# Optimization experiments

Hardware: AMD Instinct MI355X
Metric: run time of the kernel (lower is better)

The kernel has to match this reference:

```python
import jax, jax.numpy as jnp
import numpy as np

N = 4096            # nodes
LMAX = 6
NUM_COEF = (LMAX + 1) ** 2   # 49 SH coefficients
RES = 18            # S2 grid resolution (lat = lon = 18)
C = 128             # num_channels


def setup_inputs() -> dict:
    key = jax.random.key(0)
    k1, k2, k3, k4 = jax.random.split(key, 4)
    return {
        "inputs": jax.random.normal(k1, (N, NUM_COEF, 2 * C), dtype=jnp.float32),
        "scalars": jax.random.normal(k2, (N, 3 * C), dtype=jnp.float32),
        # SO3Grid projection matrices (precomputed SH-basis grids in the real module)
        "to_grid_mat": jax.random.normal(k3, (RES, RES, NUM_COEF), dtype=jnp.float32) / np.sqrt(NUM_COEF).astype(np.float32),
        "from_grid_mat": jax.random.normal(k4, (RES, RES, NUM_COEF), dtype=jnp.float32) / np.float32(RES),
    }


def reference(inputs, scalars, to_grid_mat, from_grid_mat):
    # inputs:  [N, (lmax+1)^2, 2C]; scalars: [N, 3C]
    n, k, c2 = inputs.shape
    s = scalars[:, None, :]                       # [N, 1, 3C]
    # Type-0 path part 1: SwiGLU on first 2C scalars -> [N, 1, C]
    a, b = jnp.split(s[..., :c2], 2, axis=-1)
    output_scalars = jax.nn.silu(a) * b
    # Type-0 path part 2: sigmoid gate on last C scalars -> [N, 1, C]
    gate_scalars = jax.nn.sigmoid(s[..., c2:])
    # Type-L path: project to S2 grid -> [N, RES, RES, 2C]
    x_grid = jnp.einsum('pqi,nic->npqc', to_grid_mat, inputs)
    # chunk-multiply gating (self tensor product) -> [N, RES, RES, C]
    x1, x2 = jnp.split(x_grid, 2, axis=-1)
    x_grid = x1 * x2
    # project back to SH coefficients -> [N, (lmax+1)^2, C]
    output_vectors = jnp.einsum('pqi,npqc->nic', from_grid_mat, x_grid)
    output_vectors = output_vectors * gate_scalars
    # merge: add SwiGLU scalars onto the l=0 component
    return output_vectors.at[:, 0:1, :].add(output_scalars)
```

## Files before the change

### kernel.cpp

```cpp
#include <hip/hip_runtime.h>


#define KC    49
#define PQ    324
#define NPX   12544
#define OUTK  6272
#define NTILE 11
#define TROWS 325
#define TCOLS 68
#define FROWS 50
#define FCOLS 356
#define TTOT  (TROWS * TCOLS)
#define FTOT  (FROWS * FCOLS)
#define WTOT  (TTOT + FTOT)
#define WPAD  39904

typedef __attribute__((ext_vector_type(8)))  short bf16x8;
typedef __attribute__((ext_vector_type(4)))  short bf16x4;
typedef __attribute__((ext_vector_type(16))) float f32x16;
typedef __attribute__((ext_vector_type(4)))  unsigned int u32x4;

__device__ __forceinline__ unsigned int cvtpk_bf16(float lo, float hi) {
    unsigned int r;
    asm("v_cvt_pk_bf16_f32 %0, %1, %2" : "=v"(r) : "v"(lo), "v"(hi));
    return r;
}
__device__ __forceinline__ unsigned short f2bf(float f) {
    unsigned u = __builtin_bit_cast(unsigned, f);
    return (unsigned short)((u + 0x7FFFu + ((u >> 16) & 1u)) >> 16);
}
__device__ __forceinline__ bf16x8 ld8(const unsigned short* p) {
    const bf16x4 lo = *(const bf16x4*)p;
    const bf16x4 hi = *(const bf16x4*)(p + 4);
    bf16x8 r;
    r[0] = lo[0]; r[1] = lo[1]; r[2] = lo[2]; r[3] = lo[3];
    r[4] = hi[0]; r[5] = hi[1]; r[6] = hi[2]; r[7] = hi[3];
    return r;
}
__device__ __forceinline__ void load_ch(const float* xp, int xi, int st, int hb, float* buf) {
#pragma unroll
    for (int j = 0; j < 8; ++j) {
        const int i = 16 * st + 8 * hb + j;
        buf[j] = (i < KC) ? xp[128 * xi + (size_t)i * 256] : 0.0f;
    }
}
__device__ __forceinline__ bf16x8 cvt_ch(const float* buf) {
    u32x4 d;
#pragma unroll
    for (int p = 0; p < 4; ++p) d[p] = cvtpk_bf16(buf[2 * p], buf[2 * p + 1]);
    return __builtin_bit_cast(bf16x8, d);
}

__global__ void prep_kernel(const float* __restrict__ Tg, const float* __restrict__ Fg,
                            unsigned short* __restrict__ W)
{
    const int idx = blockIdx.x * 256 + threadIdx.x;
    if (idx < TTOT) {
        const int r = idx / TCOLS, i = idx % TCOLS;
        const float v = (r < PQ && i < KC) ? Tg[r * KC + i] : 0.0f;
        W[idx] = f2bf(v);
    } else if (idx < WPAD) {
        float v = 0.0f;
        if (idx < WTOT) {
            const int idx2 = idx - TTOT;
            const int k = idx2 / FCOLS, p = idx2 % FCOLS;
            if (k < KC && p < PQ) v = Fg[p * KC + k];
        }
        W[idx] = f2bf(v);
    }
}

__global__ __launch_bounds__(512, 2)
void s2_fused(const float* __restrict__ X,
              const float* __restrict__ S,
              const unsigned short* __restrict__ W,
              float* __restrict__ out,
              int nit,
              float fzero)
{
    __shared__ __align__(16) unsigned short lds[WPAD];

    const int tid = threadIdx.x;
    for (int idx = tid; idx < WPAD / 8; idx += 512) {
        const u32x4 v = *(const u32x4*)(W + (size_t)idx * 8);
        *(u32x4*)(lds + (size_t)idx * 8) = v;
    }
    __syncthreads();

    const int w  = tid >> 6;
    const int l  = tid & 63;
    const int cl = l & 31;
    const int hb = l >> 5;
    const int cs = w >> 1;
    const int nw = w & 1;

    const unsigned short* tw  = lds;
    const unsigned short* fw0 = lds + TTOT + (size_t)cl * FCOLS;
    const unsigned short* fw1 = lds + TTOT + (size_t)min(cl + 32, KC) * FCOLS;

    f32x16 Z;
#pragma unroll
    for (int r = 0; r < 16; ++r) Z[r] = fzero;

    int ttc = (3 * w + (int)blockIdx.x) % NTILE;

    const unsigned short* twt0 = tw + (size_t)min(32 * ttc + cl, 324) * TCOLS + 8 * hb;
    bf16x8 tc0 = ld8(twt0);
    bf16x8 tc1 = ld8(twt0 + 16);
    bf16x8 tc2 = ld8(twt0 + 32);
    bf16x8 tc3 = ld8(twt0 + 48);

    const int nbase = blockIdx.x * (2 * nit) + nw;

    for (int it = 0; it < nit; ++it) {
        const int n = nbase + 2 * it;

        const float* xp = X + (size_t)n * NPX + 32 * cs + cl;
        const float* sp = S + (size_t)n * 384 + 32 * cs + cl;
        const float sraw0 = sp[0], sraw1 = sp[128], sraw2 = sp[256];
        const float sg  = 1.0f / (1.0f + __expf(-sraw2));
        const float osc = (sraw0 / (1.0f + __expf(-sraw0))) * sraw1;

        bf16x8 bx[2][4];
        {
            float r0[8], r1[8], r2[8], r3[8];
            load_ch(xp, 0, 0, hb, r0);
            load_ch(xp, 1, 0, hb, r1);
            load_ch(xp, 0, 1, hb, r2);
            load_ch(xp, 1, 1, hb, r3);
            bx[0][0] = cvt_ch(r0); load_ch(xp, 0, 2, hb, r0);
            bx[1][0] = cvt_ch(r1); load_ch(xp, 1, 2, hb, r1);
            bx[0][1] = cvt_ch(r2); load_ch(xp, 0, 3, hb, r2);
            bx[1][1] = cvt_ch(r3); load_ch(xp, 1, 3, hb, r3);
            bx[0][2] = cvt_ch(r0);
            bx[1][2] = cvt_ch(r1);
            bx[0][3] = cvt_ch(r2);
            bx[1][3] = cvt_ch(r3);
        }

        f32x16 accO0, accO1;
#pragma unroll
        for (int r = 0; r < 16; ++r) { accO0[r] = 0.0f; accO1[r] = 0.0f; }

        for (int t = 0; t < NTILE; ++t) {
            const int ttn = (ttc == NTILE - 1) ? 0 : ttc + 1;
            const unsigned short* twtN = tw + (size_t)min(32 * ttn + cl, 324) * TCOLS + 8 * hb;
            const bf16x8 nc0 = ld8(twtN);
            const bf16x8 nc1 = ld8(twtN + 16);
            const bf16x8 nc2 = ld8(twtN + 32);
            const bf16x8 nc3 = ld8(twtN + 48);

            f32x16 ac0, ac1;
            ac0 = __builtin_amdgcn_mfma_f32_32x32x16_bf16(tc0, bx[0][0], Z, 0, 0, 0);
            ac1 = __builtin_amdgcn_mfma_f32_32x32x16_bf16(tc0, bx[1][0], Z, 0, 0, 0);
            ac0 = __builtin_amdgcn_mfma_f32_32x32x16_bf16(tc1, bx[0][1], ac0, 0, 0, 0);
            ac1 = __builtin_amdgcn_mfma_f32_32x32x16_bf16(tc1, bx[1][1], ac1, 0, 0, 0);
            ac0 = __builtin_amdgcn_mfma_f32_32x32x16_bf16(tc2, bx[0][2], ac0, 0, 0, 0);
            ac1 = __builtin_amdgcn_mfma_f32_32x32x16_bf16(tc2, bx[1][2], ac1, 0, 0, 0);
            ac0 = __builtin_amdgcn_mfma_f32_32x32x16_bf16(tc3, bx[0][3], ac0, 0, 0, 0);
            ac1 = __builtin_amdgcn_mfma_f32_32x32x16_bf16(tc3, bx[1][3], ac1, 0, 0, 0);

            const int fcol = 32 * ttc + 8 * hb;
            const bf16x8 fa00 = ld8(fw0 + fcol);
            const bf16x8 fa01 = ld8(fw0 + fcol + 16);
            const bf16x8 fa10 = ld8(fw1 + fcol);
            const bf16x8 fa11 = ld8(fw1 + fcol + 16);

            unsigned int q0 = cvtpk_bf16(ac0[0]  * ac1[0],  ac0[1]  * ac1[1]);
            unsigned int q1 = cvtpk_bf16(ac0[2]  * ac1[2],  ac0[3]  * ac1[3]);
            unsigned int q2 = cvtpk_bf16(ac0[4]  * ac1[4],  ac0[5]  * ac1[5]);
            unsigned int q3 = cvtpk_bf16(ac0[6]  * ac1[6],  ac0[7]  * ac1[7]);
            unsigned int q4 = cvtpk_bf16(ac0[8]  * ac1[8],  ac0[9]  * ac1[9]);
            unsigned int q5 = cvtpk_bf16(ac0[10] * ac1[10], ac0[11] * ac1[11]);
            unsigned int q6 = cvtpk_bf16(ac0[12] * ac1[12], ac0[13] * ac1[13]);
            unsigned int q7 = cvtpk_bf16(ac0[14] * ac1[14], ac0[15] * ac1[15]);

            asm("v_permlane32_swap_b32 %0, %1" : "+v"(q0), "+v"(q2));
            asm("v_permlane32_swap_b32 %0, %1" : "+v"(q1), "+v"(q3));
            asm("v_permlane32_swap_b32 %0, %1" : "+v"(q4), "+v"(q6));
            asm("v_permlane32_swap_b32 %0, %1" : "+v"(q5), "+v"(q7));
            u32x4 b0v, b1v;
            b0v[0] = q0; b0v[1] = q1; b0v[2] = q2; b0v[3] = q3;
            b1v[0] = q4; b1v[1] = q5; b1v[2] = q6; b1v[3] = q7;
            const bf16x8 bg0 = __builtin_bit_cast(bf16x8, b0v);
            const bf16x8 bg1 = __builtin_bit_cast(bf16x8, b1v);

            accO0 = __builtin_amdgcn_mfma_f32_32x32x16_bf16(fa00, bg0, accO0, 0, 0, 0);
            accO1 = __builtin_amdgcn_mfma_f32_32x32x16_bf16(fa10, bg0, accO1, 0, 0, 0);
            accO0 = __builtin_amdgcn_mfma_f32_32x32x16_bf16(fa01, bg1, accO0, 0, 0, 0);
            accO1 = __builtin_amdgcn_mfma_f32_32x32x16_bf16(fa11, bg1, accO1, 0, 0, 0);

            tc0 = nc0; tc1 = nc1; tc2 = nc2; tc3 = nc3;
            ttc = ttn;
        }

        float* op = out + (size_t)n * OUTK + 32 * cs + cl;
#pragma unroll
        for (int r = 0; r < 16; ++r) {
            const int k0 = (r & 3) + 8 * (r >> 2) + 4 * hb;
            float v = sg * accO0[r];
            if (k0 == 0) v += osc;
            op[(size_t)k0 * 128] = v;
            const int k1 = 32 + k0;
            if (k1 < KC) op[(size_t)k1 * 128] = sg * accO1[r];
        }
    }
}

extern "C" void kernel_launch(void* const* d_in, const int* in_sizes, int n_in,
                              void* d_out, int out_size, void* d_ws, size_t ws_size,
                              hipStream_t stream) {
    const float* inputs  = (const float*)d_in[0];
    const float* scalars = (const float*)d_in[1];
    const float* Tg      = (const float*)d_in[2];
    const float* Fg      = (const float*)d_in[3];
    float* outp          = (float*)d_out;

    unsigned short* W = (unsigned short*)d_ws;

    const int N = in_sizes[1] / 384;
    hipLaunchKernelGGL(prep_kernel, dim3((WPAD + 255) / 256), dim3(256), 0, stream,
                       Tg, Fg, W);

    const int nit  = 4;
    const int grid = N / (2 * nit);
    hipLaunchKernelGGL(s2_fused, dim3(grid), dim3(512), 0, stream,
                       inputs, scalars, W, outp, nit, 0.0f);
}
```

Measured before the change: 95.21 us.

## Pre-swizzle projection weights into per-lane fragment layout for 128-bit LDS reads

The prep kernel now writes both projection matrices in the exact per-lane MFMA fragment order, so each lane fetches an operand with one contiguous 16-byte LDS load instead of two 8-byte loads from padded row-major tiles. The tile loop is fully unrolled, and the rotated tile start with software prefetch of the next tile's weights is dropped. The goal is fewer LDS instructions and bank conflicts in the inner loop. In exchange, LDS use grows from about 78 KB to 88 KB per block, and all waves now read the same tile at the same time.

Measured after the change: 95.54 us. No clear change (+0.3%).

```diff
diff --git a/kernel.cpp b/kernel.cpp
--- a/kernel.cpp
+++ b/kernel.cpp
@@ -6,17 +6,11 @@
 #define NPX   12544
 #define OUTK  6272
 #define NTILE 11
-#define TROWS 325
-#define TCOLS 68
-#define FROWS 50
-#define FCOLS 356
-#define TTOT  (TROWS * TCOLS)
-#define FTOT  (FROWS * FCOLS)
-#define WTOT  (TTOT + FTOT)
-#define WPAD  39904
+#define TFTOT 22528
+#define FFTOT 22528
+#define WTOT  (TFTOT + FFTOT)
 
 typedef __attribute__((ext_vector_type(8)))  short bf16x8;
-typedef __attribute__((ext_vector_type(4)))  short bf16x4;
 typedef __attribute__((ext_vector_type(16))) float f32x16;
 typedef __attribute__((ext_vector_type(4)))  unsigned int u32x4;
 
@@ -29,14 +23,6 @@
     unsigned u = __builtin_bit_cast(unsigned, f);
     return (unsigned short)((u + 0x7FFFu + ((u >> 16) & 1u)) >> 16);
 }
-__device__ __forceinline__ bf16x8 ld8(const unsigned short* p) {
-    const bf16x4 lo = *(const bf16x4*)p;
-    const bf16x4 hi = *(const bf16x4*)(p + 4);
-    bf16x8 r;
-    r[0] = lo[0]; r[1] = lo[1]; r[2] = lo[2]; r[3] = lo[3];
-    r[4] = hi[0]; r[5] = hi[1]; r[6] = hi[2]; r[7] = hi[3];
-    return r;
-}
 __device__ __forceinline__ void load_ch(const float* xp, int xi, int st, int hb, float* buf) {
 #pragma unroll
     for (int j = 0; j < 8; ++j) {
@@ -55,18 +41,24 @@
                             unsigned short* __restrict__ W)
 {
     const int idx = blockIdx.x * 256 + threadIdx.x;
-    if (idx < TTOT) {
-        const int r = idx / TCOLS, i = idx % TCOLS;
-        const float v = (r < PQ && i < KC) ? Tg[r * KC + i] : 0.0f;
-        W[idx] = f2bf(v);
-    } else if (idx < WPAD) {
-        float v = 0.0f;
-        if (idx < WTOT) {
-            const int idx2 = idx - TTOT;
-            const int k = idx2 / FCOLS, p = idx2 % FCOLS;
-            if (k < KC && p < PQ) v = Fg[p * KC + k];
-        }
-        W[idx] = f2bf(v);
+    if (idx < TFTOT) {
+        const int j = idx & 7;
+        const int l = (idx >> 3) & 63;
+        const int f = (idx >> 9) & 3;
+        const int t = idx >> 11;
+        const int pq = 32 * t + (l & 31);
+        const int i  = 16 * f + 8 * (l >> 5) + j;
+        W[idx] = f2bf((pq < PQ && i < KC) ? Tg[pq * KC + i] : 0.0f);
+    } else if (idx < WTOT) {
+        const int idx2 = idx - TFTOT;
+        const int j = idx2 & 7;
+        const int l = (idx2 >> 3) & 63;
+        const int h = (idx2 >> 9) & 1;
+        const int g = (idx2 >> 10) & 1;
+        const int t = idx2 >> 11;
+        const int pq = 32 * t + 16 * h + 8 * (l >> 5) + j;
+        const int k  = 32 * g + (l & 31);
+        W[idx] = f2bf((pq < PQ && k < KC) ? Fg[pq * KC + k] : 0.0f);
     }
 }
 
@@ -78,10 +70,10 @@
               int nit,
               float fzero)
 {
-    __shared__ __align__(16) unsigned short lds[WPAD];
+    __shared__ __align__(16) unsigned short lds[WTOT];
 
     const int tid = threadIdx.x;
-    for (int idx = tid; idx < WPAD / 8; idx += 512) {
+    for (int idx = tid; idx < WTOT / 8; idx += 512) {
         const u32x4 v = *(const u32x4*)(W + (size_t)idx * 8);
         *(u32x4*)(lds + (size_t)idx * 8) = v;
     }
@@ -94,21 +86,12 @@
     const int cs = w >> 1;
     const int nw = w & 1;
 
-    const unsigned short* tw  = lds;
-    const unsigned short* fw0 = lds + TTOT + (size_t)cl * FCOLS;
-    const unsigned short* fw1 = lds + TTOT + (size_t)min(cl + 32, KC) * FCOLS;
+    const unsigned short* tf = lds + (size_t)(l << 3);
+    const unsigned short* ff = tf + TFTOT;
 
     f32x16 Z;
 #pragma unroll
     for (int r = 0; r < 16; ++r) Z[r] = fzero;
-
-    int ttc = (3 * w + (int)blockIdx.x) % NTILE;
-
-    const unsigned short* twt0 = tw + (size_t)min(32 * ttc + cl, 324) * TCOLS + 8 * hb;
-    bf16x8 tc0 = ld8(twt0);
-    bf16x8 tc1 = ld8(twt0 + 16);
-    bf16x8 tc2 = ld8(twt0 + 32);
-    bf16x8 tc3 = ld8(twt0 + 48);
 
     const int nbase = blockIdx.x * (2 * nit) + nw;
 
@@ -142,29 +125,27 @@
 #pragma unroll
         for (int r = 0; r < 16; ++r) { accO0[r] = 0.0f; accO1[r] = 0.0f; }
 
+#pragma unroll
         for (int t = 0; t < NTILE; ++t) {
-            const int ttn = (ttc == NTILE - 1) ? 0 : ttc + 1;
-            const unsigned short* twtN = tw + (size_t)min(32 * ttn + cl, 324) * TCOLS + 8 * hb;
-            const bf16x8 nc0 = ld8(twtN);
-            const bf16x8 nc1 = ld8(twtN + 16);
-            const bf16x8 nc2 = ld8(twtN + 32);
-            const bf16x8 nc3 = ld8(twtN + 48);
+            const bf16x8 ta0 = *(const bf16x8*)(tf + (t * 4 + 0) * 512);
+            const bf16x8 ta1 = *(const bf16x8*)(tf + (t * 4 + 1) * 512);
+            const bf16x8 ta2 = *(const bf16x8*)(tf + (t * 4 + 2) * 512);
+            const bf16x8 ta3 = *(const bf16x8*)(tf + (t * 4 + 3) * 512);
 
             f32x16 ac0, ac1;
-            ac0 = __builtin_amdgcn_mfma_f32_32x32x16_bf16(tc0, bx[0][0], Z, 0, 0, 0);
-            ac1 = __builtin_amdgcn_mfma_f32_32x32x16_bf16(tc0, bx[1][0], Z, 0, 0, 0);
-            ac0 = __builtin_amdgcn_mfma_f32_32x32x16_bf16(tc1, bx[0][1], ac0, 0, 0, 0);
-            ac1 = __builtin_amdgcn_mfma_f32_32x32x16_bf16(tc1, bx[1][1], ac1, 0, 0, 0);
-            ac0 = __builtin_amdgcn_mfma_f32_32x32x16_bf16(tc2, bx[0][2], ac0, 0, 0, 0);
-            ac1 = __builtin_amdgcn_mfma_f32_32x32x16_bf16(tc2, bx[1][2], ac1, 0, 0, 0);
-            ac0 = __builtin_amdgcn_mfma_f32_32x32x16_bf16(tc3, bx[0][3], ac0, 0, 0, 0);
-            ac1 = __builtin_amdgcn_mfma_f32_32x32x16_bf16(tc3, bx[1][3], ac1, 0, 0, 0);
-
-            const int fcol = 32 * ttc + 8 * hb;
-            const bf16x8 fa00 = ld8(fw0 + fcol);
-            const bf16x8 fa01 = ld8(fw0 + fcol + 16);
-            const bf16x8 fa10 = ld8(fw1 + fcol);
-            const bf16x8 fa11 = ld8(fw1 + fcol + 16);
+            ac0 = __builtin_amdgcn_mfma_f32_32x32x16_bf16(ta0, bx[0][0], Z, 0, 0, 0);
+            ac1 = __builtin_amdgcn_mfma_f32_32x32x16_bf16(ta0, bx[1][0], Z, 0, 0, 0);
+            ac0 = __builtin_amdgcn_mfma_f32_32x32x16_bf16(ta1, bx[0][1], ac0, 0, 0, 0);
+            ac1 = __builtin_amdgcn_mfma_f32_32x32x16_bf16(ta1, bx[1][1], ac1, 0, 0, 0);
+            ac0 = __builtin_amdgcn_mfma_f32_32x32x16_bf16(ta2, bx[0][2], ac0, 0, 0, 0);
+            ac1 = __builtin_amdgcn_mfma_f32_32x32x16_bf16(ta2, bx[1][2], ac1, 0, 0, 0);
+            ac0 = __builtin_amdgcn_mfma_f32_32x32x16_bf16(ta3, bx[0][3], ac0, 0, 0, 0);
+            ac1 = __builtin_amdgcn_mfma_f32_32x32x16_bf16(ta3, bx[1][3], ac1, 0, 0, 0);
+
+            const bf16x8 fa00 = *(const bf16x8*)(ff + (t * 4 + 0) * 512);
+            const bf16x8 fa01 = *(const bf16x8*)(ff + (t * 4 + 1) * 512);
+            const bf16x8 fa10 = *(const bf16x8*)(ff + (t * 4 + 2) * 512);
+            const bf16x8 fa11 = *(const bf16x8*)(ff + (t * 4 + 3) * 512);
 
             unsigned int q0 = cvtpk_bf16(ac0[0]  * ac1[0],  ac0[1]  * ac1[1]);
             unsigned int q1 = cvtpk_bf16(ac0[2]  * ac1[2],  ac0[3]  * ac1[3]);
@@ -189,9 +170,6 @@
             accO1 = __builtin_amdgcn_mfma_f32_32x32x16_bf16(fa10, bg0, accO1, 0, 0, 0);
             accO0 = __builtin_amdgcn_mfma_f32_32x32x16_bf16(fa01, bg1, accO0, 0, 0, 0);
             accO1 = __builtin_amdgcn_mfma_f32_32x32x16_bf16(fa11, bg1, accO1, 0, 0, 0);
-
-            tc0 = nc0; tc1 = nc1; tc2 = nc2; tc3 = nc3;
-            ttc = ttn;
         }
 
         float* op = out + (size_t)n * OUTK + 32 * cs + cl;
@@ -219,7 +197,7 @@
     unsigned short* W = (unsigned short*)d_ws;
 
     const int N = in_sizes[1] / 384;
-    hipLaunchKernelGGL(prep_kernel, dim3((WPAD + 255) / 256), dim3(256), 0, stream,
+    hipLaunchKernelGGL(prep_kernel, dim3((WTOT + 255) / 256), dim3(256), 0, stream,
                        Tg, Fg, W);
 
     const int nit  = 4;
```
